# Performance work log

Hardware: AMD Instinct MI355X
Metric: run time of the kernel (lower is better)

Reference implementation:

```python
import jax, jax.numpy as jnp
import numpy as np

DIM = 1024
SEGMENT_SIZE = 1024
DILATION_RATE = 2

def setup_inputs() -> dict:
    key = jax.random.key(0)
    x = jax.random.normal(key, (4, 8192, DIM), dtype=jnp.float32)
    return {"x": x}

def reference(x) -> jnp.ndarray:
    B, S, D = x.shape
    pad = (-S) % SEGMENT_SIZE
    x = jnp.pad(x, ((0, 0), (0, pad), (0, 0)))
    # [B, n_seg, segment_size, D]
    x = x.reshape(B, -1, SEGMENT_SIZE, D)
    # dilation: strided slice within each segment -> [B, n_seg, seg', D]
    x = x[:, :, ::DILATION_RATE, :]
    q = k = v = x
    scale = 1.0 / jnp.sqrt(jnp.asarray(D, dtype=x.dtype))
    # attention within each segment over dilated tokens (non-causal, no dropout)
    scores = jnp.einsum('bsqd,bskd->bsqk', q, k) * scale
    probs = jax.nn.softmax(scores, axis=-1)
    attn = jnp.einsum('bsqk,bskd->bsqd', probs, v)
    # flatten segments back to a (shortened, dilated) sequence
    return attn.reshape(B, -1, D)
```

## Files before the change

kernel.cpp:

```cpp
#include <hip/hip_runtime.h>


typedef float          f32x4  __attribute__((ext_vector_type(4)));
typedef short          bf16x8 __attribute__((ext_vector_type(8)));

#define MFMA16(a, b, c) __builtin_amdgcn_mfma_f32_16x16x32_bf16((a), (b), (c), 0, 0, 0)

static __device__ __forceinline__ unsigned short f2bf(float f) {
    unsigned u = __float_as_uint(f);
    u = (u + 0x7fffu + ((u >> 16) & 1u)) >> 16;
    return (unsigned short)u;
}

static __device__ __forceinline__ void async_cp16(const unsigned short* g, unsigned short* l) {
    __builtin_amdgcn_global_load_lds((const __attribute__((address_space(1))) unsigned int*)g,
                                     (__attribute__((address_space(3))) unsigned int*)l,
                                     16, 0, 0);
}

static __device__ __forceinline__ void stage_tile(const unsigned short* __restrict__ src,
                                                  unsigned short* lds,
                                                  int row_stride, int col0,
                                                  int wave, int lane) {
    const int pr = lane >> 3;
    const int lc = (lane & 7) ^ pr;
    #pragma unroll
    for (int c = 0; c < 4; ++c) {
        const int chunk = wave * 4 + c;
        async_cp16(src + (size_t)(chunk * 8 + pr) * row_stride + col0 + lc * 8,
                   lds + chunk * 512);
    }
}

__global__ __launch_bounds__(256) void k_prep(const float* __restrict__ x,
                                              unsigned short* __restrict__ Xb,
                                              unsigned short* __restrict__ VT) {
    const int kb = blockIdx.x, db = blockIdx.y, g = blockIdx.z;
    const int t = threadIdx.x;
    __shared__ unsigned short Ts[64][72];
    {
        const int r = t >> 2, q = t & 3;
        const float* src = x + ((size_t)g << 20) + (size_t)(kb * 64 + r) * 2048 + db * 64 + q * 16;
        alignas(16) unsigned short tmp[16];
        #pragma unroll
        for (int i = 0; i < 4; ++i) {
            const float4 v = *reinterpret_cast<const float4*>(src + i * 4);
            tmp[i * 4 + 0] = f2bf(v.x); tmp[i * 4 + 1] = f2bf(v.y);
            tmp[i * 4 + 2] = f2bf(v.z); tmp[i * 4 + 3] = f2bf(v.w);
        }
        unsigned short* xb = Xb + ((size_t)g * 512 + kb * 64 + r) * 1024 + db * 64 + q * 16;
        *reinterpret_cast<uint4*>(xb)     = *reinterpret_cast<const uint4*>(&tmp[0]);
        *reinterpret_cast<uint4*>(xb + 8) = *reinterpret_cast<const uint4*>(&tmp[8]);
        *reinterpret_cast<uint4*>(&Ts[r][q * 16])     = *reinterpret_cast<const uint4*>(&tmp[0]);
        *reinterpret_cast<uint4*>(&Ts[r][q * 16 + 8]) = *reinterpret_cast<const uint4*>(&tmp[8]);
    }
    __syncthreads();
    {
        const int dl = t >> 2, kq = t & 3;
        alignas(16) unsigned short o[16];
        #pragma unroll
        for (int j = 0; j < 16; ++j) o[j] = Ts[kq * 16 + j][dl];
        unsigned short* vt = VT + ((size_t)g * 1024 + db * 64 + dl) * 512 + kb * 64 + kq * 16;
        *reinterpret_cast<uint4*>(vt)     = *reinterpret_cast<const uint4*>(&o[0]);
        *reinterpret_cast<uint4*>(vt + 8) = *reinterpret_cast<const uint4*>(&o[8]);
    }
}

__global__ __launch_bounds__(256) void k_scores(const unsigned short* __restrict__ Xb,
                                                unsigned short* __restrict__ T,
                                                float* __restrict__ Lsum) {
    const int g = blockIdx.x, nb = blockIdx.y, mb = blockIdx.z;
    const int tid = threadIdx.x, wave = tid >> 6, lane = tid & 63;
    const int g4 = lane >> 4, n16 = lane & 15;
    const int wr = wave & 1, wc = wave >> 1;

    __shared__ unsigned short As[128 * 64];
    __shared__ unsigned short Bs[128 * 64];
    __shared__ float red[4][64];

    const unsigned short* Ag = Xb + ((size_t)g * 512 + mb * 128) * 1024;
    const unsigned short* Bg = Xb + ((size_t)g * 512 + nb * 128) * 1024;

    f32x4 acc[16];
    const f32x4 vzero = {0.f, 0.f, 0.f, 0.f};
    #pragma unroll
    for (int i = 0; i < 16; ++i) acc[i] = vzero;

    for (int kt = 0; kt < 16; ++kt) {
        if (kt) __syncthreads();
        stage_tile(Ag, As, 1024, kt * 64, wave, lane);
        stage_tile(Bg, Bs, 1024, kt * 64, wave, lane);
        __syncthreads();
        #pragma unroll
        for (int ks = 0; ks < 2; ++ks) {
            const int sw = ((ks * 4 + g4) ^ (n16 & 7)) * 8;
            bf16x8 a[4], b[4];
            #pragma unroll
            for (int i = 0; i < 4; ++i)
                a[i] = *reinterpret_cast<const bf16x8*>(&As[(wr * 64 + i * 16 + n16) * 64 + sw]);
            #pragma unroll
            for (int j = 0; j < 4; ++j)
                b[j] = *reinterpret_cast<const bf16x8*>(&Bs[(wc * 64 + j * 16 + n16) * 64 + sw]);
            #pragma unroll
            for (int i = 0; i < 4; ++i)
                #pragma unroll
                for (int j = 0; j < 4; ++j)
                    acc[i * 4 + j] = MFMA16(a[i], b[j], acc[i * 4 + j]);
        }
    }

    float rs[4][4];
    #pragma unroll
    for (int i = 0; i < 4; ++i)
        #pragma unroll
        for (int r = 0; r < 4; ++r) rs[i][r] = 0.f;

    unsigned short* Tg = T + ((size_t)g * 512 + mb * 128 + wr * 64) * 512 + nb * 128 + wc * 64;
    #pragma unroll
    for (int i = 0; i < 4; ++i)
        #pragma unroll
        for (int j = 0; j < 4; ++j)
            #pragma unroll
            for (int r = 0; r < 4; ++r) {
                const float e = __expf(acc[i * 4 + j][r] * 0.03125f);
                rs[i][r] += e;
                Tg[(size_t)(i * 16 + g4 * 4 + r) * 512 + j * 16 + n16] = f2bf(e);
            }

    #pragma unroll
    for (int d = 1; d < 16; d <<= 1)
        #pragma unroll
        for (int i = 0; i < 4; ++i)
            #pragma unroll
            for (int r = 0; r < 4; ++r)
                rs[i][r] += __shfl_xor(rs[i][r], d, 64);
    if (n16 == 0) {
        #pragma unroll
        for (int i = 0; i < 4; ++i)
            #pragma unroll
            for (int r = 0; r < 4; ++r)
                red[wave][i * 16 + g4 * 4 + r] = rs[i][r];
    }
    __syncthreads();
    if (tid < 128) {
        const int h = tid >> 6, idx = tid & 63;
        atomicAdd(&Lsum[g * 512 + mb * 128 + h * 64 + idx],
                  red[h][idx] + red[h + 2][idx]);
    }
}

__global__ __launch_bounds__(256) void k_pv(const unsigned short* __restrict__ T,
                                            const unsigned short* __restrict__ VT,
                                            const float* __restrict__ Lsum,
                                            float* __restrict__ out) {
    const int g = blockIdx.x, nb = blockIdx.y, mb = blockIdx.z;
    const int tid = threadIdx.x, wave = tid >> 6, lane = tid & 63;
    const int g4 = lane >> 4, n16 = lane & 15;
    const int wr = wave & 1, wc = wave >> 1;

    __shared__ unsigned short As[128 * 64];
    __shared__ unsigned short Bs[128 * 64];
    __shared__ float Linv[128];

    if (tid < 128) Linv[tid] = 1.0f / Lsum[g * 512 + mb * 128 + tid];

    const unsigned short* Ag = T  + ((size_t)g * 512  + mb * 128) * 512;
    const unsigned short* Bg = VT + ((size_t)g * 1024 + nb * 128) * 512;

    f32x4 acc[16];
    const f32x4 vzero = {0.f, 0.f, 0.f, 0.f};
    #pragma unroll
    for (int i = 0; i < 16; ++i) acc[i] = vzero;

    for (int kt = 0; kt < 8; ++kt) {
        __syncthreads();
        stage_tile(Ag, As, 512, kt * 64, wave, lane);
        stage_tile(Bg, Bs, 512, kt * 64, wave, lane);
        __syncthreads();
        #pragma unroll
        for (int ks = 0; ks < 2; ++ks) {
            const int sw = ((ks * 4 + g4) ^ (n16 & 7)) * 8;
            bf16x8 a[4], b[4];
            #pragma unroll
            for (int i = 0; i < 4; ++i)
                a[i] = *reinterpret_cast<const bf16x8*>(&As[(wr * 64 + i * 16 + n16) * 64 + sw]);
            #pragma unroll
            for (int j = 0; j < 4; ++j)
                b[j] = *reinterpret_cast<const bf16x8*>(&Bs[(wc * 64 + j * 16 + n16) * 64 + sw]);
            #pragma unroll
            for (int i = 0; i < 4; ++i)
                #pragma unroll
                for (int j = 0; j < 4; ++j)
                    acc[i * 4 + j] = MFMA16(a[i], b[j], acc[i * 4 + j]);
        }
    }

    float li[4][4];
    #pragma unroll
    for (int i = 0; i < 4; ++i)
        #pragma unroll
        for (int r = 0; r < 4; ++r)
            li[i][r] = Linv[wr * 64 + i * 16 + g4 * 4 + r];

    float* og = out + ((size_t)g * 512 + mb * 128 + wr * 64) * 1024 + nb * 128 + wc * 64;
    #pragma unroll
    for (int i = 0; i < 4; ++i)
        #pragma unroll
        for (int j = 0; j < 4; ++j)
            #pragma unroll
            for (int r = 0; r < 4; ++r)
                og[(size_t)(i * 16 + g4 * 4 + r) * 1024 + j * 16 + n16] =
                    acc[i * 4 + j][r] * li[i][r];
}

extern "C" void kernel_launch(void* const* d_in, const int* in_sizes, int n_in,
                              void* d_out, int out_size, void* d_ws, size_t ws_size,
                              hipStream_t stream) {
    const float* x = (const float*)d_in[0];
    float* out = (float*)d_out;

    unsigned short* T  = (unsigned short*)d_ws;
    unsigned short* Xb = T  + (size_t)32 * 512 * 512;
    unsigned short* VT = Xb + (size_t)32 * 512 * 1024;
    float*          Ls = (float*)(VT + (size_t)32 * 1024 * 512);

    hipMemsetAsync(Ls, 0, 32 * 512 * sizeof(float), stream);
    k_prep  <<<dim3(8, 16, 32), 256, 0, stream>>>(x, Xb, VT);
    k_scores<<<dim3(32, 4, 4),  256, 0, stream>>>(Xb, T, Ls);
    k_pv    <<<dim3(32, 8, 4),  256, 0, stream>>>(T, VT, Ls, out);
}
```

Before: 247.5 us.

## Double-buffer LDS tiles in score and PV GEMM kernels

```diff
diff --git a/kernel.cpp b/kernel.cpp
--- a/kernel.cpp
+++ b/kernel.cpp
@@ -74,8 +74,8 @@
     const int g4 = lane >> 4, n16 = lane & 15;
     const int wr = wave & 1, wc = wave >> 1;
 
-    __shared__ unsigned short As[128 * 64];
-    __shared__ unsigned short Bs[128 * 64];
+    __shared__ unsigned short As[2][128 * 64];
+    __shared__ unsigned short Bs[2][128 * 64];
     __shared__ float red[4][64];
 
     const unsigned short* Ag = Xb + ((size_t)g * 512 + mb * 128) * 1024;
@@ -86,21 +86,26 @@
     #pragma unroll
     for (int i = 0; i < 16; ++i) acc[i] = vzero;
 
+    stage_tile(Ag, As[0], 1024, 0, wave, lane);
+    stage_tile(Bg, Bs[0], 1024, 0, wave, lane);
+
     for (int kt = 0; kt < 16; ++kt) {
-        if (kt) __syncthreads();
-        stage_tile(Ag, As, 1024, kt * 64, wave, lane);
-        stage_tile(Bg, Bs, 1024, kt * 64, wave, lane);
+        const int buf = kt & 1;
         __syncthreads();
+        if (kt + 1 < 16) {
+            stage_tile(Ag, As[buf ^ 1], 1024, (kt + 1) * 64, wave, lane);
+            stage_tile(Bg, Bs[buf ^ 1], 1024, (kt + 1) * 64, wave, lane);
+        }
         #pragma unroll
         for (int ks = 0; ks < 2; ++ks) {
             const int sw = ((ks * 4 + g4) ^ (n16 & 7)) * 8;
             bf16x8 a[4], b[4];
             #pragma unroll
             for (int i = 0; i < 4; ++i)
-                a[i] = *reinterpret_cast<const bf16x8*>(&As[(wr * 64 + i * 16 + n16) * 64 + sw]);
+                a[i] = *reinterpret_cast<const bf16x8*>(&As[buf][(wr * 64 + i * 16 + n16) * 64 + sw]);
             #pragma unroll
             for (int j = 0; j < 4; ++j)
-                b[j] = *reinterpret_cast<const bf16x8*>(&Bs[(wc * 64 + j * 16 + n16) * 64 + sw]);
+                b[j] = *reinterpret_cast<const bf16x8*>(&Bs[buf][(wc * 64 + j * 16 + n16) * 64 + sw]);
             #pragma unroll
             for (int i = 0; i < 4; ++i)
                 #pragma unroll
@@ -158,8 +163,8 @@
     const int g4 = lane >> 4, n16 = lane & 15;
     const int wr = wave & 1, wc = wave >> 1;
 
-    __shared__ unsigned short As[128 * 64];
-    __shared__ unsigned short Bs[128 * 64];
+    __shared__ unsigned short As[2][128 * 64];
+    __shared__ unsigned short Bs[2][128 * 64];
     __shared__ float Linv[128];
 
     if (tid < 128) Linv[tid] = 1.0f / Lsum[g * 512 + mb * 128 + tid];
@@ -172,21 +177,26 @@
     #pragma unroll
     for (int i = 0; i < 16; ++i) acc[i] = vzero;
 
+    stage_tile(Ag, As[0], 512, 0, wave, lane);
+    stage_tile(Bg, Bs[0], 512, 0, wave, lane);
+
     for (int kt = 0; kt < 8; ++kt) {
+        const int buf = kt & 1;
         __syncthreads();
-        stage_tile(Ag, As, 512, kt * 64, wave, lane);
-        stage_tile(Bg, Bs, 512, kt * 64, wave, lane);
-        __syncthreads();
+        if (kt + 1 < 8) {
+            stage_tile(Ag, As[buf ^ 1], 512, (kt + 1) * 64, wave, lane);
+            stage_tile(Bg, Bs[buf ^ 1], 512, (kt + 1) * 64, wave, lane);
+        }
         #pragma unroll
         for (int ks = 0; ks < 2; ++ks) {
             const int sw = ((ks * 4 + g4) ^ (n16 & 7)) * 8;
             bf16x8 a[4], b[4];
             #pragma unroll
             for (int i = 0; i < 4; ++i)
-                a[i] = *reinterpret_cast<const bf16x8*>(&As[(wr * 64 + i * 16 + n16) * 64 + sw]);
+                a[i] = *reinterpret_cast<const bf16x8*>(&As[buf][(wr * 64 + i * 16 + n16) * 64 + sw]);
             #pragma unroll
             for (int j = 0; j < 4; ++j)
-                b[j] = *reinterpret_cast<const bf16x8*>(&Bs[(wc * 64 + j * 16 + n16) * 64 + sw]);
+                b[j] = *reinterpret_cast<const bf16x8*>(&Bs[buf][(wc * 64 + j * 16 + n16) * 64 + sw]);
             #pragma unroll
             for (int i = 0; i < 4; ++i)
                 #pragma unroll
```

Measured after the change: 248.1 us. About the same (+0.3%).
